# Optimization experiments

Hardware: AMD Instinct MI355X
Metric: run time of the kernel (lower is better)

The kernel has to match this reference:

```python
import jax, jax.numpy as jnp
import numpy as np

N_NODES = 100000
DIN = 512
B = 1024
T_STEPS = 6
DOUT = 512


def setup_inputs() -> dict:
    key = jax.random.key(0)
    ks = jax.random.split(key, 8)
    s = 0.02  # small init scale for numerical sanity
    x = jax.random.normal(ks[0], (N_NODES, DIN), jnp.float32)
    batch = jnp.sort(jax.random.randint(ks[1], (N_NODES,), 0, B)).astype(jnp.int64)
    Wih = jax.random.normal(ks[2], (4 * DIN, 2 * DIN), jnp.float32) * s
    Whh = jax.random.normal(ks[3], (4 * DIN, DIN), jnp.float32) * s
    bih = jax.random.normal(ks[4], (4 * DIN,), jnp.float32) * s
    bhh = jax.random.normal(ks[5], (4 * DIN,), jnp.float32) * s
    Wpost = jax.random.normal(ks[6], (DOUT, 2 * DIN), jnp.float32) * s
    bpost = jax.random.normal(ks[7], (DOUT,), jnp.float32) * s
    return {"x": x, "batch": batch, "Wih": Wih, "Whh": Whh, "bih": bih,
            "bhh": bhh, "Wpost": Wpost, "bpost": bpost, "num_graphs": B}


def reference(x, batch, Wih, Whh, bih, bhh, Wpost, bpost, num_graphs):
    din = x.shape[1]
    Bg = num_graphs
    h = jnp.zeros((Bg, din), x.dtype)
    c = jnp.zeros((Bg, din), x.dtype)
    q_star = jnp.zeros((Bg, 2 * din), x.dtype)  # [q, r]
    for _ in range(T_STEPS):
        # single-layer LSTM cell over the "batch of graphs" axis
        z = q_star @ Wih.T + h @ Whh.T + (bih + bhh)  # [B, 4*din]
        i, f, g, o = jnp.split(z, 4, axis=-1)  # torch gate order i,f,g,o
        c = jax.nn.sigmoid(f) * c + jax.nn.sigmoid(i) * jnp.tanh(g)
        h = jax.nn.sigmoid(o) * jnp.tanh(c)
        q = h  # [B, din]
        # segment (scatter) softmax attention over nodes of each graph
        e = jnp.sum(x * q[batch], axis=-1)  # [N]
        emax = jax.ops.segment_max(e, batch, num_segments=Bg)
        ex = jnp.exp(e - emax[batch])
        denom = jax.ops.segment_sum(ex, batch, num_segments=Bg)
        a = ex / denom[batch]  # [N]
        r = jax.ops.segment_sum(a[:, None] * x, batch, num_segments=Bg)  # [B, din]
        q_star = jnp.concatenate([q, r], axis=-1)
    # post_pool: Linear(2*din -> dim_out) + bias + ReLU (dropout=0, eval mode)
    out = jax.nn.relu(q_star @ Wpost.T + bpost)
    return out
```

## Files before the change

kernel.cpp:

```cpp
#include <hip/hip_runtime.h>
#include <stdint.h>
#include <stddef.h>

#define DIN    512
#define BGR    1024
#define NGATE  2048
#define KQ     1024
#define DOUT   512
#define TSTEPS 6

typedef unsigned short ushort_t;
typedef short bf16x8 __attribute__((ext_vector_type(8)));
typedef unsigned short u16x8 __attribute__((ext_vector_type(8)));
typedef float f32x4 __attribute__((ext_vector_type(4)));

__device__ __forceinline__ float b2f(unsigned short u) {
    unsigned int i = ((unsigned int)u) << 16;
    float f;
    __builtin_memcpy(&f, &i, 4);
    return f;
}

__device__ __forceinline__ unsigned short f2b(float f) {
    unsigned int i;
    __builtin_memcpy(&i, &f, 4);
    unsigned int lsb = (i >> 16) & 1u;
    i += 0x7fffu + lsb;
    return (unsigned short)(i >> 16);
}

__device__ __forceinline__ float fast_sigmoid(float v) {
    return 1.f / (1.f + __expf(-v));
}

__device__ __forceinline__ float fast_tanh(float v) {
    float t = fabsf(v);
    float e = __expf(-2.f * t);
    float r = (1.f - e) / (1.f + e);
    return v < 0.f ? -r : r;
}

__global__ void probe_dtypes(const ushort_t* x, const ushort_t* Wih,
                             const ushort_t* Whh, const ushort_t* bih,
                             const ushort_t* bhh, const ushort_t* Wpost,
                             const ushort_t* bpost, int* flags)
{
    __shared__ int cnt[7];
    const int tid = threadIdx.x;
    if (tid < 7) cnt[tid] = 0;
    __syncthreads();
    const int t = tid >> 5;
    const int l = tid & 31;
    if (t < 7) {
        const ushort_t* p = (t == 0) ? x : (t == 1) ? Wih : (t == 2) ? Whh
                          : (t == 3) ? bih : (t == 4) ? bhh
                          : (t == 5) ? Wpost : bpost;
        int good = 0;
        for (int i = 0; i < 4; i++) {
            ushort_t u = p[(l * 4 + i) * 2];
            int ex = (u >> 7) & 0xFF;
            if (ex == 0 || (ex >= 96 && ex <= 143)) good++;
        }
        atomicAdd(&cnt[t], good);
    }
    __syncthreads();
    if (tid < 7) flags[tid] = (cnt[tid] < 96) ? 1 : 0;
}

__global__ void convert_x(const void* __restrict__ xin, ushort_t* __restrict__ xb,
                          long long T, const int* __restrict__ flags)
{
    long long i8 = ((long long)blockIdx.x * 256 + threadIdx.x) * 8;
    if (i8 >= T) return;
    if (flags[0]) {
        const float* xp = (const float*)xin;
        f32x4 v0 = *(const f32x4*)(xp + i8);
        f32x4 v1 = *(const f32x4*)(xp + i8 + 4);
        u16x8 o;
#pragma unroll
        for (int j = 0; j < 4; j++) o[j] = f2b(v0[j]);
#pragma unroll
        for (int j = 0; j < 4; j++) o[4 + j] = f2b(v1[j]);
        *(u16x8*)(xb + i8) = o;
    } else {
        *(u16x8*)(xb + i8) = *(const u16x8*)((const ushort_t*)xin + i8);
    }
}

#define BM 128
#define BN 64
#define BK 32

template <int MODE>
__global__ __launch_bounds__(256)
void gemm_bt(const ushort_t* __restrict__ Ag, const ushort_t* __restrict__ Bg,
             const float* __restrict__ bias, float* __restrict__ Cout,
             int M, int N, int K)
{
    __shared__ __align__(16) ushort_t As[BM * BK];
    __shared__ __align__(16) ushort_t Bs[BN * BK];

    const int tid  = threadIdx.x;
    const int lane = tid & 63;
    const int w    = tid >> 6;
    const int wr   = w >> 1;
    const int wc   = w & 1;
    const int lrow = lane & 15;
    const int quad = lane >> 4;

    const int n0 = blockIdx.x * BN;
    const int m0 = blockIdx.y * BM;

    const int srow = tid >> 2;
    const int scol = (tid & 3) * 8;

    f32x4 acc[4][2];
#pragma unroll
    for (int i = 0; i < 4; i++)
#pragma unroll
        for (int j = 0; j < 2; j++)
            acc[i][j] = (f32x4){0.f, 0.f, 0.f, 0.f};

    for (int kt = 0; kt < K; kt += BK) {
        bf16x8 a0v = *(const bf16x8*)(Ag + ((size_t)(m0 + srow) * K + kt + scol));
        bf16x8 a1v = *(const bf16x8*)(Ag + ((size_t)(m0 + 64 + srow) * K + kt + scol));
        bf16x8 bv  = *(const bf16x8*)(Bg + ((size_t)(n0 + srow) * K + kt + scol));
        __syncthreads();
        *(bf16x8*)&As[srow * BK + scol]        = a0v;
        *(bf16x8*)&As[(64 + srow) * BK + scol] = a1v;
        *(bf16x8*)&Bs[srow * BK + scol]        = bv;
        __syncthreads();

        bf16x8 af[4], bfr[2];
#pragma unroll
        for (int mi = 0; mi < 4; mi++)
            af[mi] = *(const bf16x8*)&As[(wr * 64 + mi * 16 + lrow) * BK + quad * 8];
#pragma unroll
        for (int ni = 0; ni < 2; ni++)
            bfr[ni] = *(const bf16x8*)&Bs[(wc * 32 + ni * 16 + lrow) * BK + quad * 8];

#pragma unroll
        for (int mi = 0; mi < 4; mi++)
#pragma unroll
            for (int ni = 0; ni < 2; ni++)
                acc[mi][ni] = __builtin_amdgcn_mfma_f32_16x16x32_bf16(
                    af[mi], bfr[ni], acc[mi][ni], 0, 0, 0);
    }

#pragma unroll
    for (int mi = 0; mi < 4; mi++) {
#pragma unroll
        for (int ni = 0; ni < 2; ni++) {
#pragma unroll
            for (int r = 0; r < 4; r++) {
                int gm = m0 + wr * 64 + mi * 16 + quad * 4 + r;
                int gn = n0 + wc * 32 + ni * 16 + lrow;
                float v = acc[mi][ni][r] + bias[gn];
                if (MODE == 1) {
                    if (!(v > 0.f) && (v == v)) v = 0.f;
                }
                Cout[(size_t)gm * N + gn] = v;
            }
        }
    }
}

template <int XMODE>
__global__ __launch_bounds__(256)
void attn_step2(const void* __restrict__ xptr, const int* __restrict__ offs,
                const float* __restrict__ z, float* __restrict__ c,
                ushort_t* __restrict__ A)
{
    const int b    = blockIdx.x;
    const int tid  = threadIdx.x;
    const int lane = tid & 63;
    const int w    = tid >> 6;

    __shared__ float qsh[DIN];
    __shared__ float accL[4][DIN];
    __shared__ float mw[4], lw[4];

    const float* zrow = z + (size_t)b * NGATE;
    for (int d = tid; d < DIN; d += 256) {
        float zi = zrow[d];
        float zf = zrow[DIN + d];
        float zg = zrow[2 * DIN + d];
        float zo = zrow[3 * DIN + d];
        float cc = c[(size_t)b * DIN + d];
        cc = fast_sigmoid(zf) * cc + fast_sigmoid(zi) * fast_tanh(zg);
        float hh = fast_sigmoid(zo) * fast_tanh(cc);
        c[(size_t)b * DIN + d] = cc;
        A[(size_t)b * KQ + d]  = f2b(hh);
        qsh[d] = hh;
    }
    __syncthreads();

    const int s  = offs[b];
    const int en = offs[b + 1];

    float q8[8];
#pragma unroll
    for (int j = 0; j < 8; j++) q8[j] = qsh[lane * 8 + j];

    const float NEG_INF = -__builtin_inff();
    float m = NEG_INF, l = 0.f;
    float acc[8];
#pragma unroll
    for (int j = 0; j < 8; j++) acc[j] = 0.f;

    auto load_row = [&](int n, float* xf) {
        if (XMODE == 0) {
            u16x8 xv = *(const u16x8*)((const ushort_t*)xptr + (size_t)n * DIN + lane * 8);
#pragma unroll
            for (int j = 0; j < 8; j++) xf[j] = b2f(xv[j]);
        } else {
            const float* xp = (const float*)xptr;
            f32x4 v0 = *(const f32x4*)(xp + (size_t)n * DIN + lane * 8);
            f32x4 v1 = *(const f32x4*)(xp + (size_t)n * DIN + lane * 8 + 4);
#pragma unroll
            for (int j = 0; j < 4; j++) { xf[j] = v0[j]; xf[4 + j] = v1[j]; }
        }
    };

    float xf[8];
    int n = s + w;
    if (n < en) load_row(n, xf);
    for (; n < en; n += 4) {
        float xn[8];
        const int nn = n + 4;
        if (nn < en) load_row(nn, xn);

        float e = 0.f;
#pragma unroll
        for (int j = 0; j < 8; j++) e += q8[j] * xf[j];
#pragma unroll
        for (int off = 32; off > 0; off >>= 1) e += __shfl_xor(e, off, 64);

        float mn_   = fmaxf(m, e);
        float alpha = __expf(m - mn_);
        float pp    = __expf(e - mn_);
        l = l * alpha + pp;
#pragma unroll
        for (int j = 0; j < 8; j++) acc[j] = acc[j] * alpha + pp * xf[j];
        m = mn_;

#pragma unroll
        for (int j = 0; j < 8; j++) xf[j] = xn[j];
    }

    if (lane == 0) { mw[w] = m; lw[w] = l; }
#pragma unroll
    for (int j = 0; j < 8; j++) accL[w][lane * 8 + j] = acc[j];
    __syncthreads();

    const float M = fmaxf(fmaxf(mw[0], mw[1]), fmaxf(mw[2], mw[3]));
    const int d0 = tid * 2;
    float r0 = 0.f, r1 = 0.f, lt = 0.f;
#pragma unroll
    for (int ww = 0; ww < 4; ww++) {
        float mwv = mw[ww];
        float a = (mwv == NEG_INF) ? 0.f : __expf(mwv - M);
        lt += a * lw[ww];
        r0 += a * accL[ww][d0];
        r1 += a * accL[ww][d0 + 1];
    }
    float inv = lt > 0.f ? 1.f / lt : 0.f;
    A[(size_t)b * KQ + DIN + d0]     = f2b(r0 * inv);
    A[(size_t)b * KQ + DIN + d0 + 1] = f2b(r1 * inv);
}

__global__ void prep_weights(const ushort_t* __restrict__ Wih,
                             const ushort_t* __restrict__ Whh,
                             const ushort_t* __restrict__ bih,
                             const ushort_t* __restrict__ bhh,
                             const ushort_t* __restrict__ Wpost,
                             const ushort_t* __restrict__ bpost,
                             ushort_t* __restrict__ Wp,
                             float* __restrict__ biasz,
                             float* __restrict__ biaspost,
                             ushort_t* __restrict__ Wpb,
                             const int* __restrict__ flags)
{
    const int idx = blockIdx.x * 256 + threadIdx.x;
    const int fWih = flags[1], fWhh = flags[2], fbih = flags[3];
    const int fbhh = flags[4], fWpo = flags[5], fbpo = flags[6];

    if (idx < NGATE * KQ) {
        int j = idx >> 10;
        int k = idx & 1023;
        float v = fWih ? ((const float*)Wih)[idx] : b2f(Wih[idx]);
        if (k < DIN) {
            int widx = j * DIN + k;
            v += fWhh ? ((const float*)Whh)[widx] : b2f(Whh[widx]);
        }
        Wp[idx] = f2b(v);
    }
    if (idx < DOUT * KQ) {
        Wpb[idx] = fWpo ? f2b(((const float*)Wpost)[idx]) : Wpost[idx];
    }
    if (idx < NGATE) {
        float v1 = fbih ? ((const float*)bih)[idx] : b2f(bih[idx]);
        float v2 = fbhh ? ((const float*)bhh)[idx] : b2f(bhh[idx]);
        biasz[idx] = v1 + v2;
    }
    if (idx < DOUT) {
        biaspost[idx] = fbpo ? ((const float*)bpost)[idx] : b2f(bpost[idx]);
    }
}

__global__ void prep_state(ushort_t* __restrict__ A, float* __restrict__ c)
{
    int idx = blockIdx.x * 256 + threadIdx.x;
    if (idx < BGR * KQ)  A[idx] = 0;
    if (idx < BGR * DIN) c[idx] = 0.f;
}

__global__ void prep_offsets(const int* __restrict__ batch, int* __restrict__ offs, int Nn)
{
    int n = blockIdx.x * 256 + threadIdx.x;
    if (n >= Nn) return;
    const bool is64 = batch[Nn - 1] < batch[Nn - 2];
    int cur  = is64 ? batch[2 * n] : batch[n];
    int prev = (n == 0) ? -1 : (is64 ? batch[2 * (n - 1)] : batch[n - 1]);
    for (int bb = prev + 1; bb <= cur; ++bb) offs[bb] = n;
    if (n == Nn - 1) {
        for (int bb = cur + 1; bb <= BGR; ++bb) offs[bb] = Nn;
    }
}

extern "C" void kernel_launch(void* const* d_in, const int* in_sizes, int n_in,
                              void* d_out, int out_size, void* d_ws, size_t ws_size,
                              hipStream_t stream)
{
    const ushort_t* x     = (const ushort_t*)d_in[0];
    const int*      batch = (const int*)d_in[1];
    const ushort_t* Wih   = (const ushort_t*)d_in[2];
    const ushort_t* Whh   = (const ushort_t*)d_in[3];
    const ushort_t* bih   = (const ushort_t*)d_in[4];
    const ushort_t* bhh   = (const ushort_t*)d_in[5];
    const ushort_t* Wpost = (const ushort_t*)d_in[6];
    const ushort_t* bpost = (const ushort_t*)d_in[7];
    const int Nn = in_sizes[1];
    const long long Tx = (long long)in_sizes[0];

    char* p = (char*)d_ws;
    auto carve = [&](size_t bytes) -> void* {
        char* q = p;
        p += (bytes + 255) & ~(size_t)255;
        return (void*)q;
    };
    ushort_t* Wp       = (ushort_t*)carve((size_t)NGATE * KQ * 2);
    ushort_t* Wpb      = (ushort_t*)carve((size_t)DOUT * KQ * 2);
    float*    biasz    = (float*)carve((size_t)NGATE * 4);
    float*    biaspost = (float*)carve((size_t)DOUT * 4);
    float*    z        = (float*)carve((size_t)BGR * NGATE * 4);
    float*    c        = (float*)carve((size_t)BGR * DIN * 4);
    ushort_t* A        = (ushort_t*)carve((size_t)BGR * KQ * 2);
    int*      offs     = (int*)carve((size_t)(BGR + 1) * 4);
    int*      flags    = (int*)carve(16 * 4);
    size_t used = (size_t)(p - (char*)d_ws);
    const bool use_xb = (ws_size >= used + (size_t)Tx * 2 + 256);
    ushort_t* xb = use_xb ? (ushort_t*)carve((size_t)Tx * 2) : nullptr;

    probe_dtypes<<<1, 256, 0, stream>>>(x, Wih, Whh, bih, bhh, Wpost, bpost, flags);
    prep_weights<<<(NGATE * KQ) / 256, 256, 0, stream>>>(
        Wih, Whh, bih, bhh, Wpost, bpost, Wp, biasz, biaspost, Wpb, flags);
    prep_state<<<(BGR * KQ) / 256, 256, 0, stream>>>(A, c);
    prep_offsets<<<(Nn + 255) / 256, 256, 0, stream>>>(batch, offs, Nn);
    if (use_xb) {
        int cblocks = (int)((Tx / 8 + 255) / 256);
        convert_x<<<cblocks, 256, 0, stream>>>(x, xb, Tx, flags);
    }

    for (int t = 0; t < TSTEPS; ++t) {
        gemm_bt<0><<<dim3(NGATE / BN, BGR / BM), 256, 0, stream>>>(
            A, Wp, biasz, z, BGR, NGATE, KQ);
        if (use_xb)
            attn_step2<0><<<BGR, 256, 0, stream>>>(xb, offs, z, c, A);
        else
            attn_step2<1><<<BGR, 256, 0, stream>>>(x, offs, z, c, A);
    }
    gemm_bt<1><<<dim3(DOUT / BN, BGR / BM), 256, 0, stream>>>(
        A, Wpb, biaspost, (float*)d_out, BGR, DOUT, KQ);
}
```

Baseline: 631.2 us.

## Fuse x bf16 conversion into first attention step, shrink GEMM tile, unroll node loop

Drops the separate convert_x pass: the first attention step reads raw x, uses it directly and writes the bf16 copy for later steps. This saves one full extra read of x. The gate GEMM tile is halved in M (128 to 64) so more blocks are launched for the 1024x2048 output. The node loop now processes two rows per wave per iteration, which adds memory-level parallelism but also raises register pressure.

Measured after the change: 571.2 us. 9.5% less time.

```diff
diff --git a/kernel.cpp b/kernel.cpp
--- a/kernel.cpp
+++ b/kernel.cpp
@@ -67,27 +67,7 @@
     if (tid < 7) flags[tid] = (cnt[tid] < 96) ? 1 : 0;
 }
 
-__global__ void convert_x(const void* __restrict__ xin, ushort_t* __restrict__ xb,
-                          long long T, const int* __restrict__ flags)
-{
-    long long i8 = ((long long)blockIdx.x * 256 + threadIdx.x) * 8;
-    if (i8 >= T) return;
-    if (flags[0]) {
-        const float* xp = (const float*)xin;
-        f32x4 v0 = *(const f32x4*)(xp + i8);
-        f32x4 v1 = *(const f32x4*)(xp + i8 + 4);
-        u16x8 o;
-#pragma unroll
-        for (int j = 0; j < 4; j++) o[j] = f2b(v0[j]);
-#pragma unroll
-        for (int j = 0; j < 4; j++) o[4 + j] = f2b(v1[j]);
-        *(u16x8*)(xb + i8) = o;
-    } else {
-        *(u16x8*)(xb + i8) = *(const u16x8*)((const ushort_t*)xin + i8);
-    }
-}
-
-#define BM 128
+#define BM 64
 #define BN 64
 #define BK 32
 
@@ -114,33 +94,31 @@
     const int srow = tid >> 2;
     const int scol = (tid & 3) * 8;
 
-    f32x4 acc[4][2];
-#pragma unroll
-    for (int i = 0; i < 4; i++)
+    f32x4 acc[2][2];
+#pragma unroll
+    for (int i = 0; i < 2; i++)
 #pragma unroll
         for (int j = 0; j < 2; j++)
             acc[i][j] = (f32x4){0.f, 0.f, 0.f, 0.f};
 
     for (int kt = 0; kt < K; kt += BK) {
-        bf16x8 a0v = *(const bf16x8*)(Ag + ((size_t)(m0 + srow) * K + kt + scol));
-        bf16x8 a1v = *(const bf16x8*)(Ag + ((size_t)(m0 + 64 + srow) * K + kt + scol));
-        bf16x8 bv  = *(const bf16x8*)(Bg + ((size_t)(n0 + srow) * K + kt + scol));
+        bf16x8 av = *(const bf16x8*)(Ag + ((size_t)(m0 + srow) * K + kt + scol));
+        bf16x8 bv = *(const bf16x8*)(Bg + ((size_t)(n0 + srow) * K + kt + scol));
         __syncthreads();
-        *(bf16x8*)&As[srow * BK + scol]        = a0v;
-        *(bf16x8*)&As[(64 + srow) * BK + scol] = a1v;
-        *(bf16x8*)&Bs[srow * BK + scol]        = bv;
+        *(bf16x8*)&As[srow * BK + scol] = av;
+        *(bf16x8*)&Bs[srow * BK + scol] = bv;
         __syncthreads();
 
-        bf16x8 af[4], bfr[2];
-#pragma unroll
-        for (int mi = 0; mi < 4; mi++)
-            af[mi] = *(const bf16x8*)&As[(wr * 64 + mi * 16 + lrow) * BK + quad * 8];
+        bf16x8 af[2], bfr[2];
+#pragma unroll
+        for (int mi = 0; mi < 2; mi++)
+            af[mi] = *(const bf16x8*)&As[(wr * 32 + mi * 16 + lrow) * BK + quad * 8];
 #pragma unroll
         for (int ni = 0; ni < 2; ni++)
             bfr[ni] = *(const bf16x8*)&Bs[(wc * 32 + ni * 16 + lrow) * BK + quad * 8];
 
 #pragma unroll
-        for (int mi = 0; mi < 4; mi++)
+        for (int mi = 0; mi < 2; mi++)
 #pragma unroll
             for (int ni = 0; ni < 2; ni++)
                 acc[mi][ni] = __builtin_amdgcn_mfma_f32_16x16x32_bf16(
@@ -148,12 +126,12 @@
     }
 
 #pragma unroll
-    for (int mi = 0; mi < 4; mi++) {
+    for (int mi = 0; mi < 2; mi++) {
 #pragma unroll
         for (int ni = 0; ni < 2; ni++) {
 #pragma unroll
             for (int r = 0; r < 4; r++) {
-                int gm = m0 + wr * 64 + mi * 16 + quad * 4 + r;
+                int gm = m0 + wr * 32 + mi * 16 + quad * 4 + r;
                 int gn = n0 + wc * 32 + ni * 16 + lrow;
                 float v = acc[mi][ni][r] + bias[gn];
                 if (MODE == 1) {
@@ -167,14 +145,16 @@
 
 template <int XMODE>
 __global__ __launch_bounds__(256)
-void attn_step2(const void* __restrict__ xptr, const int* __restrict__ offs,
-                const float* __restrict__ z, float* __restrict__ c,
-                ushort_t* __restrict__ A)
+void attn_step(const ushort_t* __restrict__ xbsrc, const ushort_t* __restrict__ xraw,
+               ushort_t* __restrict__ xbdst, const int* __restrict__ offs,
+               const float* __restrict__ z, float* __restrict__ c,
+               ushort_t* __restrict__ A, const int* __restrict__ flags)
 {
     const int b    = blockIdx.x;
     const int tid  = threadIdx.x;
     const int lane = tid & 63;
     const int w    = tid >> 6;
+    const int xf   = (XMODE == 0) ? 0 : flags[0];
 
     __shared__ float qsh[DIN];
     __shared__ float accL[4][DIN];
@@ -208,44 +188,63 @@
 #pragma unroll
     for (int j = 0; j < 8; j++) acc[j] = 0.f;
 
-    auto load_row = [&](int n, float* xf) {
-        if (XMODE == 0) {
-            u16x8 xv = *(const u16x8*)((const ushort_t*)xptr + (size_t)n * DIN + lane * 8);
-#pragma unroll
-            for (int j = 0; j < 8; j++) xf[j] = b2f(xv[j]);
+    auto load_row = [&](int n, float* v) {
+        if (XMODE == 0 || !xf) {
+            const ushort_t* src = (XMODE == 0) ? xbsrc : xraw;
+            u16x8 xv = *(const u16x8*)(src + (size_t)n * DIN + lane * 8);
+#pragma unroll
+            for (int j = 0; j < 8; j++) v[j] = b2f(xv[j]);
+            if (XMODE == 1)
+                *(u16x8*)(xbdst + (size_t)n * DIN + lane * 8) = xv;
         } else {
-            const float* xp = (const float*)xptr;
+            const float* xp = (const float*)xraw;
             f32x4 v0 = *(const f32x4*)(xp + (size_t)n * DIN + lane * 8);
             f32x4 v1 = *(const f32x4*)(xp + (size_t)n * DIN + lane * 8 + 4);
 #pragma unroll
-            for (int j = 0; j < 4; j++) { xf[j] = v0[j]; xf[4 + j] = v1[j]; }
+            for (int j = 0; j < 4; j++) { v[j] = v0[j]; v[4 + j] = v1[j]; }
+            if (XMODE == 1) {
+                u16x8 o;
+#pragma unroll
+                for (int j = 0; j < 8; j++) o[j] = f2b(v[j]);
+                *(u16x8*)(xbdst + (size_t)n * DIN + lane * 8) = o;
+            }
         }
     };
 
-    float xf[8];
+    auto update = [&](float e, const float* xv) {
+        float mn = fmaxf(m, e);
+        float al = __expf(m - mn);
+        float pp = __expf(e - mn);
+        l = l * al + pp;
+#pragma unroll
+        for (int j = 0; j < 8; j++) acc[j] = acc[j] * al + pp * xv[j];
+        m = mn;
+    };
+
+    float xa[8] = {0.f}, xc[8] = {0.f};
     int n = s + w;
-    if (n < en) load_row(n, xf);
-    for (; n < en; n += 4) {
-        float xn[8];
-        const int nn = n + 4;
-        if (nn < en) load_row(nn, xn);
-
-        float e = 0.f;
-#pragma unroll
-        for (int j = 0; j < 8; j++) e += q8[j] * xf[j];
-#pragma unroll
-        for (int off = 32; off > 0; off >>= 1) e += __shfl_xor(e, off, 64);
-
-        float mn_   = fmaxf(m, e);
-        float alpha = __expf(m - mn_);
-        float pp    = __expf(e - mn_);
-        l = l * alpha + pp;
-#pragma unroll
-        for (int j = 0; j < 8; j++) acc[j] = acc[j] * alpha + pp * xf[j];
-        m = mn_;
-
-#pragma unroll
-        for (int j = 0; j < 8; j++) xf[j] = xn[j];
+    if (n < en)     load_row(n, xa);
+    if (n + 4 < en) load_row(n + 4, xc);
+    for (; n < en; n += 8) {
+        float pa[8], pc[8];
+        const int np = n + 8;
+        if (np < en)     load_row(np, pa);
+        if (np + 4 < en) load_row(np + 4, pc);
+
+        float e1 = 0.f, e2 = 0.f;
+#pragma unroll
+        for (int j = 0; j < 8; j++) { e1 += q8[j] * xa[j]; e2 += q8[j] * xc[j]; }
+#pragma unroll
+        for (int off = 32; off > 0; off >>= 1) {
+            e1 += __shfl_xor(e1, off, 64);
+            e2 += __shfl_xor(e2, off, 64);
+        }
+
+        update(e1, xa);
+        if (n + 4 < en) update(e2, xc);
+
+#pragma unroll
+        for (int j = 0; j < 8; j++) { xa[j] = pa[j]; xc[j] = pc[j]; }
     }
 
     if (lane == 0) { mw[w] = m; lw[w] = l; }
@@ -367,18 +366,18 @@
         Wih, Whh, bih, bhh, Wpost, bpost, Wp, biasz, biaspost, Wpb, flags);
     prep_state<<<(BGR * KQ) / 256, 256, 0, stream>>>(A, c);
     prep_offsets<<<(Nn + 255) / 256, 256, 0, stream>>>(batch, offs, Nn);
-    if (use_xb) {
-        int cblocks = (int)((Tx / 8 + 255) / 256);
-        convert_x<<<cblocks, 256, 0, stream>>>(x, xb, Tx, flags);
-    }
 
     for (int t = 0; t < TSTEPS; ++t) {
         gemm_bt<0><<<dim3(NGATE / BN, BGR / BM), 256, 0, stream>>>(
             A, Wp, biasz, z, BGR, NGATE, KQ);
-        if (use_xb)
-            attn_step2<0><<<BGR, 256, 0, stream>>>(xb, offs, z, c, A);
-        else
-            attn_step2<1><<<BGR, 256, 0, stream>>>(x, offs, z, c, A);
+        if (use_xb) {
+            if (t == 0)
+                attn_step<1><<<BGR, 256, 0, stream>>>(xb, x, xb, offs, z, c, A, flags);
+            else
+                attn_step<0><<<BGR, 256, 0, stream>>>(xb, x, xb, offs, z, c, A, flags);
+        } else {
+            attn_step<2><<<BGR, 256, 0, stream>>>(x, x, nullptr, offs, z, c, A, flags);
+        }
     }
     gemm_bt<1><<<dim3(DOUT / BN, BGR / BM), 256, 0, stream>>>(
         A, Wpb, biaspost, (float*)d_out, BGR, DOUT, KQ);
```
